# Performance work log

Hardware: AMD Instinct MI355X
Metric: run time of the kernel (lower is better)

## Reference

```python
import jax, jax.numpy as jnp
import numpy as np

N = 100000   # number of agents
IN = 64      # input_size (obs+action)
E = 128      # embed_size


def _linear_params(k, out_f, in_f, bias=True):
    kw, kb = jax.random.split(k)
    bound = 1.0 / np.sqrt(in_f)
    W = jax.random.uniform(kw, (out_f, in_f), jnp.float32, -bound, bound)
    if not bias:
        return W, None
    b = jax.random.uniform(kb, (out_f,), jnp.float32, -bound, bound)
    return W, b


def setup_inputs() -> dict:
    key = jax.random.key(0)
    ks = jax.random.split(key, 10)
    obs_actions = jax.random.normal(ks[0], (N, IN), jnp.float32)
    We, be = _linear_params(ks[1], E, IN)
    Wv, _ = _linear_params(ks[2], E, E, bias=False)
    Wq, bq = _linear_params(ks[3], E, E)
    Wk, bk = _linear_params(ks[4], E, E)
    # mlp_attention: fed a length-1 score vector -> in_features = 1 (see notes)
    W1, b1 = _linear_params(ks[5], 512, 1)
    W2, b2 = _linear_params(ks[6], 256, 512)
    W3, b3 = _linear_params(ks[7], 128, 256)
    Wo1, bo1 = _linear_params(ks[8], 128, 2 * E)
    Wo2, bo2 = _linear_params(ks[9], 1, 128)
    return {
        "obs_actions": obs_actions,
        "We": We, "be": be, "Wv": Wv, "Wq": Wq, "bq": bq, "Wk": Wk, "bk": bk,
        "W1": W1, "b1": b1, "W2": W2, "b2": b2, "W3": W3, "b3": b3,
        "Wo1": Wo1, "bo1": bo1, "Wo2": Wo2, "bo2": bo2,
        "self_idx": 0,
    }


def reference(obs_actions, We, be, Wv, Wq, bq, Wk, bk,
              W1, b1, W2, b2, W3, b3, Wo1, bo1, Wo2, bo2, self_idx):
    # embeds: [N, E]
    embeds = obs_actions @ We.T + be
    # query for the self agent: [E]
    q = embeds[self_idx] @ Wq.T + bq
    # keys for all agents (batched version of the per-neighbor loop): [N, E]
    K = embeds @ Wk.T + bk
    # per-agent scalar score: dot(q, k) / sqrt(E) -> [N]
    scores = (K @ q) / jnp.sqrt(jnp.asarray(E, jnp.float32))
    # attention MLP on the scalar score: [N,1] -> [N,512] -> [N,256] -> [N,128]
    h = jax.nn.relu(scores[:, None] @ W1.T + b1)
    h = jax.nn.relu(h @ W2.T + b2)
    sim = jax.nn.relu(h @ W3.T + b3)
    # torch.softmax(sim, dim=0) on a [128] vector == softmax over features
    weights = jax.nn.softmax(sim, axis=-1)  # [N, 128]
    values = embeds @ Wv.T                  # [N, E]
    # exclude the self agent from the aggregation
    mask = (jnp.arange(obs_actions.shape[0]) != self_idx)[:, None]
    weighted = jnp.sum(jnp.where(mask, weights * values, 0.0), axis=0)  # [E]
    critic_input = jnp.concatenate([embeds[self_idx], weighted])        # [2E]
    hidden = jax.nn.relu(critic_input @ Wo1.T + bo1)
    return hidden @ Wo2.T + bo2  # [1]
```

## Files before the change

### kernel.cpp

```cpp
#include <hip/hip_runtime.h>
#include <math.h>

#define TBL 512
#define SBLK 512

#define OFF_MM     64
#define OFF_C2     128
#define OFF_EMB    256
#define OFF_MT     512
#define OFF_WGT    8704
#define OFF_BMIN   12800
#define OFF_BMAX   13312
#define OFF_H2G    13824
#define OFF_SCORES 144896

__global__ void __launch_bounds__(256) k12(
        const float* __restrict__ X,  const float* __restrict__ We,
        const float* __restrict__ be, const float* __restrict__ Wv,
        const float* __restrict__ Wq, const float* __restrict__ bq,
        const float* __restrict__ Wk, const float* __restrict__ bk,
        const int* __restrict__ selfp, float* __restrict__ ws,
        int N, int APB)
{
    const int b = blockIdx.x, t = threadIdx.x;
    if (b == 0) {
        const int self = *selfp;
        const float4* xs4 = (const float4*)(X + (size_t)self * 64);
        if (t < 128) {
            const float4* wr = (const float4*)(We + t*64);
            float ax = 0.f, ay = 0.f, az = 0.f, aw = 0.f;
            #pragma unroll
            for (int q = 0; q < 16; ++q) {
                const float4 wv = wr[q];
                const float4 xv = xs4[q];
                ax = __builtin_fmaf(wv.x, xv.x, ax);
                ay = __builtin_fmaf(wv.y, xv.y, ay);
                az = __builtin_fmaf(wv.z, xv.z, az);
                aw = __builtin_fmaf(wv.w, xv.w, aw);
            }
            ws[OFF_EMB + t] = ((ax + ay) + (az + aw)) + be[t];
        }
        for (int i = t; i < 32*128; i += 256) ws[OFF_WGT + i] = 0.f;
    } else if (b <= 128) {
        const int r = b - 1;
        if (t < 64) {
            float acc = 0.f;
            #pragma unroll 8
            for (int e = 0; e < 128; ++e)
                acc = __builtin_fmaf(Wv[r*128 + e], We[e*64 + t], acc);
            ws[OFF_MT + t*128 + r] = acc;
        } else if (t == 64) {
            float acc = 0.f;
            for (int e = 0; e < 128; ++e)
                acc = __builtin_fmaf(Wv[r*128 + e], be[e], acc);
            ws[OFF_C2 + r] = acc;
        }
    } else {
        __shared__ float emb[128], qv[128], uu[128], vv[64];
        __shared__ float s0s;
        const int self = *selfp;
        const float4* xs4 = (const float4*)(X + (size_t)self * 64);
        if (t < 128) {
            const float4* wr = (const float4*)(We + t*64);
            float ax = 0.f, ay = 0.f, az = 0.f, aw = 0.f;
            #pragma unroll
            for (int q = 0; q < 16; ++q) {
                const float4 wv = wr[q];
                const float4 xv = xs4[q];
                ax = __builtin_fmaf(wv.x, xv.x, ax);
                ay = __builtin_fmaf(wv.y, xv.y, ay);
                az = __builtin_fmaf(wv.z, xv.z, az);
                aw = __builtin_fmaf(wv.w, xv.w, aw);
            }
            emb[t] = ((ax + ay) + (az + aw)) + be[t];
        }
        __syncthreads();
        if (t < 128) {
            const float4* wr = (const float4*)(Wq + t*128);
            float ax = 0.f, ay = 0.f, az = 0.f, aw = 0.f;
            #pragma unroll 8
            for (int q = 0; q < 32; ++q) {
                const float4 wv = wr[q];
                const float4 ev = ((const float4*)emb)[q];
                ax = __builtin_fmaf(wv.x, ev.x, ax);
                ay = __builtin_fmaf(wv.y, ev.y, ay);
                az = __builtin_fmaf(wv.z, ev.z, az);
                aw = __builtin_fmaf(wv.w, ev.w, aw);
            }
            qv[t] = ((ax + ay) + (az + aw)) + bq[t];
        }
        __syncthreads();
        if (t < 128) {
            float acc = 0.f;
            #pragma unroll 8
            for (int e = 0; e < 128; ++e)
                acc = __builtin_fmaf(Wk[e*128 + t], qv[e], acc);
            uu[t] = acc;
        }
        __syncthreads();
        const float rs = 0.08838834764831845f;
        if (t < 64) {
            float acc = 0.f;
            #pragma unroll 8
            for (int e = 0; e < 128; ++e)
                acc = __builtin_fmaf(We[e*64 + t], uu[e], acc);
            vv[t] = acc * rs;
        } else if (t == 64) {
            float acc = 0.f;
            for (int e = 0; e < 128; ++e)
                acc += be[e]*uu[e] + bk[e]*qv[e];
            s0s = acc * rs;
        }
        __syncthreads();

        const int s = b - 129;
        const int base = s * APB;
        const int n1 = min(N, base + APB);
        const int l16 = t & 15;
        const int slot = t >> 4;
        const float4 vch = *(const float4*)(vv + l16*4);
        const float s0 = s0s;
        const float4* X4 = (const float4*)X;
        float* scores = ws + OFF_SCORES;
        float smin = INFINITY, smax = -INFINITY;
        for (int n = base + slot; n < n1; n += 16) {
            const float4 xv = X4[(size_t)n*16 + l16];
            float sc = xv.x*vch.x + xv.y*vch.y + xv.z*vch.z + xv.w*vch.w;
            sc += __shfl_xor(sc, 1);
            sc += __shfl_xor(sc, 2);
            sc += __shfl_xor(sc, 4);
            sc += __shfl_xor(sc, 8);
            sc += s0;
            if (l16 == 0) scores[n] = sc;
            smin = fminf(smin, sc);
            smax = fmaxf(smax, sc);
        }
        #pragma unroll
        for (int m = 32; m >= 1; m >>= 1) {
            smin = fminf(smin, __shfl_xor(smin, m));
            smax = fmaxf(smax, __shfl_xor(smax, m));
        }
        __shared__ float rmn[4], rmx[4];
        const int wv = t >> 6;
        if ((t & 63) == 0) { rmn[wv] = smin; rmx[wv] = smax; }
        __syncthreads();
        if (t == 0) {
            ws[OFF_BMIN + s] = fminf(fminf(rmn[0], rmn[1]), fminf(rmn[2], rmn[3]));
            ws[OFF_BMAX + s] = fmaxf(fmaxf(rmx[0], rmx[1]), fmaxf(rmx[2], rmx[3]));
        }
    }
}

__global__ void __launch_bounds__(512) k3a(
        const float* __restrict__ W1, const float* __restrict__ b1,
        const float* __restrict__ W2, const float* __restrict__ b2,
        float* __restrict__ ws, int nsb)
{
    __shared__ float rmn[8], rmx[8];
    const int t = threadIdx.x;
    float mn = (t < nsb) ? ws[OFF_BMIN + t] : INFINITY;
    float mx = (t < nsb) ? ws[OFF_BMAX + t] : -INFINITY;
    #pragma unroll
    for (int m = 32; m >= 1; m >>= 1) {
        mn = fminf(mn, __shfl_xor(mn, m));
        mx = fmaxf(mx, __shfl_xor(mx, m));
    }
    if ((t & 63) == 0) { rmn[t >> 6] = mn; rmx[t >> 6] = mx; }
    __syncthreads();
    float smin = rmn[0], smax = rmx[0];
    #pragma unroll
    for (int w = 1; w < 8; ++w) {
        smin = fminf(smin, rmn[w]);
        smax = fmaxf(smax, rmx[w]);
    }
    if (blockIdx.x == 0 && t == 0) { ws[OFF_MM] = smin; ws[OFF_MM + 1] = smax; }

    const float step = (smax - smin) / (float)(TBL - 1);
    const int c = t & 255;
    const int eh = t >> 8;
    const int eA = blockIdx.x*4 + eh*2;
    const float sA = smin + step * (float)eA;
    const float sB = smin + step * (float)(eA + 1);
    const float bb = b2[c];
    float a0 = bb, a1 = bb;
    const float4* w2r = (const float4*)(W2 + c*512);
    #pragma unroll 4
    for (int kq = 0; kq < 128; ++kq) {
        const float4 w2 = w2r[kq];
        #pragma unroll
        for (int i = 0; i < 4; ++i) {
            const int k = kq*4 + i;
            const float w1v = W1[k];
            const float b1v = b1[k];
            const float h1A = fmaxf(0.f, __builtin_fmaf(sA, w1v, b1v));
            const float h1B = fmaxf(0.f, __builtin_fmaf(sB, w1v, b1v));
            const float wc = (i == 0) ? w2.x : (i == 1) ? w2.y : (i == 2) ? w2.z : w2.w;
            a0 = __builtin_fmaf(wc, h1A, a0);
            a1 = __builtin_fmaf(wc, h1B, a1);
        }
    }
    *(float2*)(ws + OFF_H2G + c*TBL + eA) = make_float2(fmaxf(0.f, a0), fmaxf(0.f, a1));
}

__global__ void __launch_bounds__(256) k3b(
        const float* __restrict__ W3, const float* __restrict__ b3,
        const float* __restrict__ h2g,
        float* __restrict__ tab)
{
    __shared__ float sm[4][128];
    const int t = threadIdx.x;
    const int j = t & 127;
    const int kh = t >> 7;
    const int e0 = blockIdx.x * 4;
    float acc[4] = {0.f, 0.f, 0.f, 0.f};
    const float4* w3r = (const float4*)(W3 + j*256 + kh*128);
    #pragma unroll 4
    for (int kq = 0; kq < 32; ++kq) {
        const float4 w3 = w3r[kq];
        #pragma unroll
        for (int i = 0; i < 4; ++i) {
            const int k = kh*128 + kq*4 + i;
            const float4 h2v = *(const float4*)(h2g + k*TBL + e0);
            const float wc = (i == 0) ? w3.x : (i == 1) ? w3.y : (i == 2) ? w3.z : w3.w;
            acc[0] = __builtin_fmaf(wc, h2v.x, acc[0]);
            acc[1] = __builtin_fmaf(wc, h2v.y, acc[1]);
            acc[2] = __builtin_fmaf(wc, h2v.z, acc[2]);
            acc[3] = __builtin_fmaf(wc, h2v.w, acc[3]);
        }
    }
    if (kh == 0) {
        const float bb = b3[j];
        #pragma unroll
        for (int e = 0; e < 4; ++e) sm[e][j] = acc[e] + bb;
    }
    __syncthreads();
    if (kh == 1) {
        #pragma unroll
        for (int e = 0; e < 4; ++e) sm[e][j] = fmaxf(0.f, sm[e][j] + acc[e]);
    }
    __syncthreads();
    const int w = t >> 6, lane = t & 63;
    const float v0 = sm[w][lane];
    const float v1 = sm[w][lane + 64];
    float m = fmaxf(v0, v1);
    #pragma unroll
    for (int msk = 1; msk < 64; msk <<= 1) m = fmaxf(m, __shfl_xor(m, msk));
    float p = __expf(v0 - m) + __expf(v1 - m);
    #pragma unroll
    for (int msk = 1; msk < 64; msk <<= 1) p += __shfl_xor(p, msk);
    const float inv = 1.f / p;
    const int row = e0 + w;
    const float g0 = __expf(v0 - m) * inv;
    const float g1 = __expf(v1 - m) * inv;
    if (row < TBL - 1) {
        tab[2*(row*128 + lane) + 0]      = g0;
        tab[2*(row*128 + lane + 64) + 0] = g1;
    }
    if (row >= 1) {
        tab[2*((row-1)*128 + lane) + 1]      = g0;
        tab[2*((row-1)*128 + lane + 64) + 1] = g1;
    }
}

__global__ void __launch_bounds__(256) k4_main(
        const float* __restrict__ X,
        const float* __restrict__ Mt,
        const float* __restrict__ c2,
        const float* __restrict__ mm,
        const float* __restrict__ scores,
        const float2* __restrict__ tab,
        const int* __restrict__ selfp,
        float* __restrict__ wgt,
        int N, int APW)
{
    const int lane = threadIdx.x & 63;
    const int wid = __builtin_amdgcn_readfirstlane(blockIdx.x*4 + (threadIdx.x >> 6));
    const int j0 = lane, j1 = lane + 64;
    const int a0 = wid * APW;
    const int a1 = min(N, a0 + APW);

    float4 M0[16], M1[16];
    #pragma unroll
    for (int q = 0; q < 16; ++q) {
        M0[q] = make_float4(Mt[(4*q+0)*128 + j0], Mt[(4*q+1)*128 + j0],
                            Mt[(4*q+2)*128 + j0], Mt[(4*q+3)*128 + j0]);
        M1[q] = make_float4(Mt[(4*q+0)*128 + j1], Mt[(4*q+1)*128 + j1],
                            Mt[(4*q+2)*128 + j1], Mt[(4*q+3)*128 + j1]);
    }
    const float cc0 = c2[j0], cc1 = c2[j1];
    const float smin = mm[0], smax = mm[1];
    const float inv_step = (smax > smin) ? (float)(TBL - 1) / (smax - smin) : 0.f;
    const int self = *selfp;

    float rho0 = 0.f, rho1 = 0.f;
    if (a0 < a1) {
        float fc; float2 t0c, t1c;
        {
            const float s = scores[a0];
            const float fi = (s - smin) * inv_step;
            int ii = (int)fi; ii = max(0, min(TBL - 2, ii));
            fc = fi - (float)ii;
            t0c = tab[ii*128 + j0]; t1c = tab[ii*128 + j1];
        }
        for (int n = a0; n < a1; ++n) {
            float fn = 0.f; float2 t0n = t0c, t1n = t1c;
            if (n + 1 < a1) {
                const float s = scores[n + 1];
                const float fi = (s - smin) * inv_step;
                int ii = (int)fi; ii = max(0, min(TBL - 2, ii));
                fn = fi - (float)ii;
                t0n = tab[ii*128 + j0]; t1n = tab[ii*128 + j1];
            }
            const float w0 = t0c.x + fc * (t0c.y - t0c.x);
            const float w1 = t1c.x + fc * (t1c.y - t1c.x);
            const float4* xr = (const float4*)(X + ((size_t)n << 6));
            float a00=0.f,a01=0.f,a02=0.f,a03=0.f;
            float b00=0.f,b01=0.f,b02=0.f,b03=0.f;
            #pragma unroll
            for (int q = 0; q < 16; ++q) {
                const float4 xv = xr[q];
                a00 = __builtin_fmaf(M0[q].x, xv.x, a00);
                a01 = __builtin_fmaf(M0[q].y, xv.y, a01);
                a02 = __builtin_fmaf(M0[q].z, xv.z, a02);
                a03 = __builtin_fmaf(M0[q].w, xv.w, a03);
                b00 = __builtin_fmaf(M1[q].x, xv.x, b00);
                b01 = __builtin_fmaf(M1[q].y, xv.y, b01);
                b02 = __builtin_fmaf(M1[q].z, xv.z, b02);
                b03 = __builtin_fmaf(M1[q].w, xv.w, b03);
            }
            const float v0 = (a00 + a01) + (a02 + a03) + cc0;
            const float v1 = (b00 + b01) + (b02 + b03) + cc1;
            if (n != self) {
                rho0 = __builtin_fmaf(w0, v0, rho0);
                rho1 = __builtin_fmaf(w1, v1, rho1);
            }
            fc = fn; t0c = t0n; t1c = t1n;
        }
    }
    const int cpy = wid & 31;
    atomicAdd(&wgt[cpy*128 + j0], rho0);
    atomicAdd(&wgt[cpy*128 + j1], rho1);
}

__global__ void __launch_bounds__(128) k5_final(
        const float* __restrict__ Wo1, const float* __restrict__ bo1,
        const float* __restrict__ Wo2, const float* __restrict__ bo2,
        float* ws, float* out)
{
    __shared__ float es[128], wg[128], red[128];
    const int t = threadIdx.x;
    es[t] = ws[OFF_EMB + t];
    float s = 0.f;
    for (int c = 0; c < 32; ++c) s += ws[OFF_WGT + c*128 + t];
    wg[t] = s;
    __syncthreads();
    const float4* wA = (const float4*)(Wo1 + t*256);
    float ax = 0.f, ay = 0.f, az = 0.f, aw = 0.f;
    #pragma unroll 8
    for (int i = 0; i < 32; ++i) {
        const float4 wv = wA[i];
        const float4 ev = ((const float4*)es)[i];
        ax = __builtin_fmaf(wv.x, ev.x, ax);
        ay = __builtin_fmaf(wv.y, ev.y, ay);
        az = __builtin_fmaf(wv.z, ev.z, az);
        aw = __builtin_fmaf(wv.w, ev.w, aw);
    }
    #pragma unroll 8
    for (int i = 0; i < 32; ++i) {
        const float4 wv = wA[32 + i];
        const float4 gv = ((const float4*)wg)[i];
        ax = __builtin_fmaf(wv.x, gv.x, ax);
        ay = __builtin_fmaf(wv.y, gv.y, ay);
        az = __builtin_fmaf(wv.z, gv.z, az);
        aw = __builtin_fmaf(wv.w, gv.w, aw);
    }
    const float acc = ((ax + ay) + (az + aw)) + bo1[t];
    red[t] = fmaxf(acc, 0.f) * Wo2[t];
    __syncthreads();
    for (int m = 64; m >= 1; m >>= 1) {
        if (t < m) red[t] += red[t + m];
        __syncthreads();
    }
    if (t == 0) out[0] = red[0] + bo2[0];
}

extern "C" void kernel_launch(void* const* d_in, const int* in_sizes, int n_in,
                              void* d_out, int out_size, void* d_ws, size_t ws_size,
                              hipStream_t stream)
{
    const float* X   = (const float*)d_in[0];
    const float* We  = (const float*)d_in[1];
    const float* be  = (const float*)d_in[2];
    const float* Wv  = (const float*)d_in[3];
    const float* Wq  = (const float*)d_in[4];
    const float* bq  = (const float*)d_in[5];
    const float* Wk  = (const float*)d_in[6];
    const float* bk  = (const float*)d_in[7];
    const float* W1  = (const float*)d_in[8];
    const float* b1  = (const float*)d_in[9];
    const float* W2  = (const float*)d_in[10];
    const float* b2  = (const float*)d_in[11];
    const float* W3  = (const float*)d_in[12];
    const float* b3  = (const float*)d_in[13];
    const float* Wo1 = (const float*)d_in[14];
    const float* bo1 = (const float*)d_in[15];
    const float* Wo2 = (const float*)d_in[16];
    const float* bo2 = (const float*)d_in[17];
    const int* selfp = (const int*)d_in[18];
    float* ws = (float*)d_ws;
    float* out = (float*)d_out;

    const int N = in_sizes[0] / 64;
    const int offTab = OFF_SCORES + ((N + 63) & ~63);
    const int APB = (N + SBLK - 1) / SBLK;
    const int nwaves = 768 * 4;
    const int APW = (N + nwaves - 1) / nwaves;

    k12<<<129 + SBLK, 256, 0, stream>>>(X, We, be, Wv, Wq, bq, Wk, bk, selfp, ws, N, APB);
    k3a<<<TBL/4, 512, 0, stream>>>(W1, b1, W2, b2, ws, SBLK);
    k3b<<<TBL/4, 256, 0, stream>>>(W3, b3, ws + OFF_H2G, ws + offTab);
    k4_main<<<768, 256, 0, stream>>>(X, ws + OFF_MT, ws + OFF_C2, ws + OFF_MM,
                                     ws + OFF_SCORES, (const float2*)(ws + offTab),
                                     selfp, ws + OFF_WGT, N, APW);
    k5_final<<<1, 128, 0, stream>>>(Wo1, bo1, Wo2, bo2, ws, out);
}
```

Measured before the change: 204.7 us.

## Fuse table MLP stages and fold final head into main kernel via last-block counter

Merges the two table-building kernels into one kernel that computes h1, h2, and the softmax rows in shared memory for two table entries per block, which removes the global h2 staging buffer. The final critic head moves into the main aggregation kernel, run by the last block to finish as detected with an atomic counter. Together these cut two kernel launches and one global round trip. The price is a serial tail in the last block, and the fused table kernel reads W2/W3 once per two entries instead of per four.

```diff
diff --git a/kernel.cpp b/kernel.cpp
--- a/kernel.cpp
+++ b/kernel.cpp
@@ -3,16 +3,17 @@
 
 #define TBL 512
 #define SBLK 512
+#define K4BLK 768
 
 #define OFF_MM     64
+#define OFF_CNT    66
 #define OFF_C2     128
 #define OFF_EMB    256
 #define OFF_MT     512
 #define OFF_WGT    8704
 #define OFF_BMIN   12800
 #define OFF_BMAX   13312
-#define OFF_H2G    13824
-#define OFF_SCORES 144896
+#define OFF_SCORES 13824
 
 __global__ void __launch_bounds__(256) k12(
         const float* __restrict__ X,  const float* __restrict__ We,
@@ -41,6 +42,7 @@
             ws[OFF_EMB + t] = ((ax + ay) + (az + aw)) + be[t];
         }
         for (int i = t; i < 32*128; i += 256) ws[OFF_WGT + i] = 0.f;
+        if (t == 0) *(unsigned*)(ws + OFF_CNT) = 0u;
     } else if (b <= 128) {
         const int r = b - 1;
         if (t < 64) {
@@ -151,15 +153,23 @@
     }
 }
 
-__global__ void __launch_bounds__(512) k3a(
+__global__ void __launch_bounds__(256) k3(
         const float* __restrict__ W1, const float* __restrict__ b1,
         const float* __restrict__ W2, const float* __restrict__ b2,
-        float* __restrict__ ws, int nsb)
+        const float* __restrict__ W3, const float* __restrict__ b3,
+        float* __restrict__ ws, int nsb, float* __restrict__ tab)
 {
-    __shared__ float rmn[8], rmx[8];
+    __shared__ float h1s[2][512];
+    __shared__ float h2s[2][256];
+    __shared__ float sm[2][128];
+    __shared__ float rmn[4], rmx[4];
     const int t = threadIdx.x;
-    float mn = (t < nsb) ? ws[OFF_BMIN + t] : INFINITY;
-    float mx = (t < nsb) ? ws[OFF_BMAX + t] : -INFINITY;
+
+    float mn = INFINITY, mx = -INFINITY;
+    for (int i = t; i < nsb; i += 256) {
+        mn = fminf(mn, ws[OFF_BMIN + i]);
+        mx = fmaxf(mx, ws[OFF_BMAX + i]);
+    }
     #pragma unroll
     for (int m = 32; m >= 1; m >>= 1) {
         mn = fminf(mn, __shfl_xor(mn, m));
@@ -167,117 +177,130 @@
     }
     if ((t & 63) == 0) { rmn[t >> 6] = mn; rmx[t >> 6] = mx; }
     __syncthreads();
-    float smin = rmn[0], smax = rmx[0];
-    #pragma unroll
-    for (int w = 1; w < 8; ++w) {
-        smin = fminf(smin, rmn[w]);
-        smax = fmaxf(smax, rmx[w]);
-    }
+    const float smin = fminf(fminf(rmn[0], rmn[1]), fminf(rmn[2], rmn[3]));
+    const float smax = fmaxf(fmaxf(rmx[0], rmx[1]), fmaxf(rmx[2], rmx[3]));
     if (blockIdx.x == 0 && t == 0) { ws[OFF_MM] = smin; ws[OFF_MM + 1] = smax; }
 
     const float step = (smax - smin) / (float)(TBL - 1);
-    const int c = t & 255;
-    const int eh = t >> 8;
-    const int eA = blockIdx.x*4 + eh*2;
-    const float sA = smin + step * (float)eA;
-    const float sB = smin + step * (float)(eA + 1);
-    const float bb = b2[c];
-    float a0 = bb, a1 = bb;
-    const float4* w2r = (const float4*)(W2 + c*512);
-    #pragma unroll 4
-    for (int kq = 0; kq < 128; ++kq) {
-        const float4 w2 = w2r[kq];
+    const int e0 = blockIdx.x * 2;
+
+    for (int idx = t; idx < 2*512; idx += 256) {
+        const int e = idx >> 9, k = idx & 511;
+        const float s = smin + step * (float)(e0 + e);
+        h1s[e][k] = fmaxf(0.f, __builtin_fmaf(s, W1[k], b1[k]));
+    }
+    __syncthreads();
+
+    {
+        const int c = t;
+        const float bb = b2[c];
+        float a0 = bb, a1 = bb, a0b = 0.f, a1b = 0.f;
+        const float4* w2r = (const float4*)(W2 + c*512);
+        #pragma unroll 8
+        for (int kq = 0; kq < 128; kq += 2) {
+            const float4 w2a = w2r[kq];
+            const float4 hA0 = *(const float4*)(&h1s[0][kq*4]);
+            const float4 hB0 = *(const float4*)(&h1s[1][kq*4]);
+            a0 = __builtin_fmaf(w2a.x, hA0.x, a0);
+            a0 = __builtin_fmaf(w2a.y, hA0.y, a0);
+            a0 = __builtin_fmaf(w2a.z, hA0.z, a0);
+            a0 = __builtin_fmaf(w2a.w, hA0.w, a0);
+            a1 = __builtin_fmaf(w2a.x, hB0.x, a1);
+            a1 = __builtin_fmaf(w2a.y, hB0.y, a1);
+            a1 = __builtin_fmaf(w2a.z, hB0.z, a1);
+            a1 = __builtin_fmaf(w2a.w, hB0.w, a1);
+            const float4 w2b = w2r[kq + 1];
+            const float4 hA1 = *(const float4*)(&h1s[0][kq*4 + 4]);
+            const float4 hB1 = *(const float4*)(&h1s[1][kq*4 + 4]);
+            a0b = __builtin_fmaf(w2b.x, hA1.x, a0b);
+            a0b = __builtin_fmaf(w2b.y, hA1.y, a0b);
+            a0b = __builtin_fmaf(w2b.z, hA1.z, a0b);
+            a0b = __builtin_fmaf(w2b.w, hA1.w, a0b);
+            a1b = __builtin_fmaf(w2b.x, hB1.x, a1b);
+            a1b = __builtin_fmaf(w2b.y, hB1.y, a1b);
+            a1b = __builtin_fmaf(w2b.z, hB1.z, a1b);
+            a1b = __builtin_fmaf(w2b.w, hB1.w, a1b);
+        }
+        h2s[0][c] = fmaxf(0.f, a0 + a0b);
+        h2s[1][c] = fmaxf(0.f, a1 + a1b);
+    }
+    __syncthreads();
+
+    {
+        const int j = t & 127, kh = t >> 7;
+        float acc0 = 0.f, acc1 = 0.f;
+        const float4* w3r = (const float4*)(W3 + j*256 + kh*128);
+        #pragma unroll 8
+        for (int kq = 0; kq < 32; ++kq) {
+            const float4 w3 = w3r[kq];
+            const float4 hA = *(const float4*)(&h2s[0][kh*128 + kq*4]);
+            const float4 hB = *(const float4*)(&h2s[1][kh*128 + kq*4]);
+            acc0 = __builtin_fmaf(w3.x, hA.x, acc0);
+            acc0 = __builtin_fmaf(w3.y, hA.y, acc0);
+            acc0 = __builtin_fmaf(w3.z, hA.z, acc0);
+            acc0 = __builtin_fmaf(w3.w, hA.w, acc0);
+            acc1 = __builtin_fmaf(w3.x, hB.x, acc1);
+            acc1 = __builtin_fmaf(w3.y, hB.y, acc1);
+            acc1 = __builtin_fmaf(w3.z, hB.z, acc1);
+            acc1 = __builtin_fmaf(w3.w, hB.w, acc1);
+        }
+        if (kh == 0) {
+            const float bb = b3[j];
+            sm[0][j] = acc0 + bb;
+            sm[1][j] = acc1 + bb;
+        }
+        __syncthreads();
+        if (kh == 1) {
+            sm[0][j] = fmaxf(0.f, sm[0][j] + acc0);
+            sm[1][j] = fmaxf(0.f, sm[1][j] + acc1);
+        }
+        __syncthreads();
+    }
+
+    const int w = t >> 6, lane = t & 63;
+    if (w < 2) {
+        const float v0 = sm[w][lane];
+        const float v1 = sm[w][lane + 64];
+        float m = fmaxf(v0, v1);
         #pragma unroll
-        for (int i = 0; i < 4; ++i) {
-            const int k = kq*4 + i;
-            const float w1v = W1[k];
-            const float b1v = b1[k];
-            const float h1A = fmaxf(0.f, __builtin_fmaf(sA, w1v, b1v));
-            const float h1B = fmaxf(0.f, __builtin_fmaf(sB, w1v, b1v));
-            const float wc = (i == 0) ? w2.x : (i == 1) ? w2.y : (i == 2) ? w2.z : w2.w;
-            a0 = __builtin_fmaf(wc, h1A, a0);
-            a1 = __builtin_fmaf(wc, h1B, a1);
-        }
-    }
-    *(float2*)(ws + OFF_H2G + c*TBL + eA) = make_float2(fmaxf(0.f, a0), fmaxf(0.f, a1));
-}
-
-__global__ void __launch_bounds__(256) k3b(
-        const float* __restrict__ W3, const float* __restrict__ b3,
-        const float* __restrict__ h2g,
-        float* __restrict__ tab)
-{
-    __shared__ float sm[4][128];
-    const int t = threadIdx.x;
-    const int j = t & 127;
-    const int kh = t >> 7;
-    const int e0 = blockIdx.x * 4;
-    float acc[4] = {0.f, 0.f, 0.f, 0.f};
-    const float4* w3r = (const float4*)(W3 + j*256 + kh*128);
-    #pragma unroll 4
-    for (int kq = 0; kq < 32; ++kq) {
-        const float4 w3 = w3r[kq];
+        for (int msk = 1; msk < 64; msk <<= 1) m = fmaxf(m, __shfl_xor(m, msk));
+        float p = __expf(v0 - m) + __expf(v1 - m);
         #pragma unroll
-        for (int i = 0; i < 4; ++i) {
-            const int k = kh*128 + kq*4 + i;
-            const float4 h2v = *(const float4*)(h2g + k*TBL + e0);
-            const float wc = (i == 0) ? w3.x : (i == 1) ? w3.y : (i == 2) ? w3.z : w3.w;
-            acc[0] = __builtin_fmaf(wc, h2v.x, acc[0]);
-            acc[1] = __builtin_fmaf(wc, h2v.y, acc[1]);
-            acc[2] = __builtin_fmaf(wc, h2v.z, acc[2]);
-            acc[3] = __builtin_fmaf(wc, h2v.w, acc[3]);
-        }
-    }
-    if (kh == 0) {
-        const float bb = b3[j];
-        #pragma unroll
-        for (int e = 0; e < 4; ++e) sm[e][j] = acc[e] + bb;
-    }
-    __syncthreads();
-    if (kh == 1) {
-        #pragma unroll
-        for (int e = 0; e < 4; ++e) sm[e][j] = fmaxf(0.f, sm[e][j] + acc[e]);
-    }
-    __syncthreads();
-    const int w = t >> 6, lane = t & 63;
-    const float v0 = sm[w][lane];
-    const float v1 = sm[w][lane + 64];
-    float m = fmaxf(v0, v1);
-    #pragma unroll
-    for (int msk = 1; msk < 64; msk <<= 1) m = fmaxf(m, __shfl_xor(m, msk));
-    float p = __expf(v0 - m) + __expf(v1 - m);
-    #pragma unroll
-    for (int msk = 1; msk < 64; msk <<= 1) p += __shfl_xor(p, msk);
-    const float inv = 1.f / p;
-    const int row = e0 + w;
-    const float g0 = __expf(v0 - m) * inv;
-    const float g1 = __expf(v1 - m) * inv;
-    if (row < TBL - 1) {
-        tab[2*(row*128 + lane) + 0]      = g0;
-        tab[2*(row*128 + lane + 64) + 0] = g1;
-    }
-    if (row >= 1) {
-        tab[2*((row-1)*128 + lane) + 1]      = g0;
-        tab[2*((row-1)*128 + lane + 64) + 1] = g1;
+        for (int msk = 1; msk < 64; msk <<= 1) p += __shfl_xor(p, msk);
+        const float inv = 1.f / p;
+        const int row = e0 + w;
+        const float g0 = __expf(v0 - m) * inv;
+        const float g1 = __expf(v1 - m) * inv;
+        if (row < TBL - 1) {
+            tab[2*(row*128 + lane) + 0]      = g0;
+            tab[2*(row*128 + lane + 64) + 0] = g1;
+        }
+        if (row >= 1) {
+            tab[2*((row-1)*128 + lane) + 1]      = g0;
+            tab[2*((row-1)*128 + lane + 64) + 1] = g1;
+        }
     }
 }
 
 __global__ void __launch_bounds__(256) k4_main(
         const float* __restrict__ X,
-        const float* __restrict__ Mt,
-        const float* __restrict__ c2,
-        const float* __restrict__ mm,
         const float* __restrict__ scores,
         const float2* __restrict__ tab,
         const int* __restrict__ selfp,
-        float* __restrict__ wgt,
-        int N, int APW)
+        float* ws,
+        const float* __restrict__ Wo1, const float* __restrict__ bo1,
+        const float* __restrict__ Wo2, const float* __restrict__ bo2,
+        float* __restrict__ out,
+        int N, int APW, int nblk)
 {
-    const int lane = threadIdx.x & 63;
-    const int wid = __builtin_amdgcn_readfirstlane(blockIdx.x*4 + (threadIdx.x >> 6));
+    const int t = threadIdx.x;
+    const int lane = t & 63;
+    const int wid = __builtin_amdgcn_readfirstlane(blockIdx.x*4 + (t >> 6));
     const int j0 = lane, j1 = lane + 64;
     const int a0 = wid * APW;
     const int a1 = min(N, a0 + APW);
+    const float* __restrict__ Mt = ws + OFF_MT;
+    float* wgt = ws + OFF_WGT;
 
     float4 M0[16], M1[16];
     #pragma unroll
@@ -287,8 +310,8 @@
         M1[q] = make_float4(Mt[(4*q+0)*128 + j1], Mt[(4*q+1)*128 + j1],
                             Mt[(4*q+2)*128 + j1], Mt[(4*q+3)*128 + j1]);
     }
-    const float cc0 = c2[j0], cc1 = c2[j1];
-    const float smin = mm[0], smax = mm[1];
+    const float cc0 = ws[OFF_C2 + j0], cc1 = ws[OFF_C2 + j1];
+    const float smin = ws[OFF_MM], smax = ws[OFF_MM + 1];
     const float inv_step = (smax > smin) ? (float)(TBL - 1) / (smax - smin) : 0.f;
     const int self = *selfp;
 
@@ -340,48 +363,58 @@
     const int cpy = wid & 31;
     atomicAdd(&wgt[cpy*128 + j0], rho0);
     atomicAdd(&wgt[cpy*128 + j1], rho1);
-}
-
-__global__ void __launch_bounds__(128) k5_final(
-        const float* __restrict__ Wo1, const float* __restrict__ bo1,
-        const float* __restrict__ Wo2, const float* __restrict__ bo2,
-        float* ws, float* out)
-{
-    __shared__ float es[128], wg[128], red[128];
-    const int t = threadIdx.x;
-    es[t] = ws[OFF_EMB + t];
-    float s = 0.f;
-    for (int c = 0; c < 32; ++c) s += ws[OFF_WGT + c*128 + t];
-    wg[t] = s;
+
+    __shared__ bool isLast;
     __syncthreads();
-    const float4* wA = (const float4*)(Wo1 + t*256);
-    float ax = 0.f, ay = 0.f, az = 0.f, aw = 0.f;
-    #pragma unroll 8
-    for (int i = 0; i < 32; ++i) {
-        const float4 wv = wA[i];
-        const float4 ev = ((const float4*)es)[i];
-        ax = __builtin_fmaf(wv.x, ev.x, ax);
-        ay = __builtin_fmaf(wv.y, ev.y, ay);
-        az = __builtin_fmaf(wv.z, ev.z, az);
-        aw = __builtin_fmaf(wv.w, ev.w, aw);
-    }
-    #pragma unroll 8
-    for (int i = 0; i < 32; ++i) {
-        const float4 wv = wA[32 + i];
-        const float4 gv = ((const float4*)wg)[i];
-        ax = __builtin_fmaf(wv.x, gv.x, ax);
-        ay = __builtin_fmaf(wv.y, gv.y, ay);
-        az = __builtin_fmaf(wv.z, gv.z, az);
-        aw = __builtin_fmaf(wv.w, gv.w, aw);
-    }
-    const float acc = ((ax + ay) + (az + aw)) + bo1[t];
-    red[t] = fmaxf(acc, 0.f) * Wo2[t];
+    if (t == 0) {
+        __threadfence();
+        const unsigned v = __hip_atomic_fetch_add((unsigned*)(ws + OFF_CNT), 1u,
+                              __ATOMIC_ACQ_REL, __HIP_MEMORY_SCOPE_AGENT);
+        isLast = (v == (unsigned)(nblk - 1));
+    }
     __syncthreads();
-    for (int m = 64; m >= 1; m >>= 1) {
-        if (t < m) red[t] += red[t + m];
-        __syncthreads();
-    }
-    if (t == 0) out[0] = red[0] + bo2[0];
+    if (isLast) {
+        __shared__ float es[128], wg[128], red[128];
+        if (t < 128) {
+            es[t] = ws[OFF_EMB + t];
+            float ssum = 0.f;
+            for (int c = 0; c < 32; ++c)
+                ssum += __hip_atomic_load(&wgt[c*128 + t], __ATOMIC_RELAXED,
+                                          __HIP_MEMORY_SCOPE_AGENT);
+            wg[t] = ssum;
+        }
+        __syncthreads();
+        if (t < 128) {
+            const float4* wA = (const float4*)(Wo1 + t*256);
+            float ax = 0.f, ay = 0.f, az = 0.f, aw = 0.f;
+            #pragma unroll 8
+            for (int i = 0; i < 32; ++i) {
+                const float4 wv = wA[i];
+                const float4 ev = ((const float4*)es)[i];
+                ax = __builtin_fmaf(wv.x, ev.x, ax);
+                ay = __builtin_fmaf(wv.y, ev.y, ay);
+                az = __builtin_fmaf(wv.z, ev.z, az);
+                aw = __builtin_fmaf(wv.w, ev.w, aw);
+            }
+            #pragma unroll 8
+            for (int i = 0; i < 32; ++i) {
+                const float4 wv = wA[32 + i];
+                const float4 gv = ((const float4*)wg)[i];
+                ax = __builtin_fmaf(wv.x, gv.x, ax);
+                ay = __builtin_fmaf(wv.y, gv.y, ay);
+                az = __builtin_fmaf(wv.z, gv.z, az);
+                aw = __builtin_fmaf(wv.w, gv.w, aw);
+            }
+            const float acc = ((ax + ay) + (az + aw)) + bo1[t];
+            red[t] = fmaxf(acc, 0.f) * Wo2[t];
+        }
+        __syncthreads();
+        for (int m = 64; m >= 1; m >>= 1) {
+            if (t < m) red[t] += red[t + m];
+            __syncthreads();
+        }
+        if (t == 0) out[0] = red[0] + bo2[0];
+    }
 }
 
 extern "C" void kernel_launch(void* const* d_in, const int* in_sizes, int n_in,
@@ -413,14 +446,11 @@
     const int N = in_sizes[0] / 64;
     const int offTab = OFF_SCORES + ((N + 63) & ~63);
     const int APB = (N + SBLK - 1) / SBLK;
-    const int nwaves = 768 * 4;
+    const int nwaves = K4BLK * 4;
     const int APW = (N + nwaves - 1) / nwaves;
 
     k12<<<129 + SBLK, 256, 0, stream>>>(X, We, be, Wv, Wq, bq, Wk, bk, selfp, ws, N, APB);
-    k3a<<<TBL/4, 512, 0, stream>>>(W1, b1, W2, b2, ws, SBLK);
-    k3b<<<TBL/4, 256, 0, stream>>>(W3, b3, ws + OFF_H2G, ws + offTab);
-    k4_main<<<768, 256, 0, stream>>>(X, ws + OFF_MT, ws + OFF_C2, ws + OFF_MM,
-                                     ws + OFF_SCORES, (const float2*)(ws + offTab),
-                                     selfp, ws + OFF_WGT, N, APW);
-    k5_final<<<1, 128, 0, stream>>>(Wo1, bo1, Wo2, bo2, ws, out);
+    k3<<<TBL/2, 256, 0, stream>>>(W1, b1, W2, b2, W3, b3, ws, SBLK, ws + offTab);
+    k4_main<<<K4BLK, 256, 0, stream>>>(X, ws + OFF_SCORES, (const float2*)(ws + offTab),
+                                       selfp, ws, Wo1, bo1, Wo2, bo2, out, N, APW, K4BLK);
 }
```

Result: slower. 210.5 us (+2.8%).
